# Performance work log

Measured on AMD Instinct MI355X. Metric: run time of the kernel, lower is better.

## Reference

```python
import jax, jax.numpy as jnp
import numpy as np

N_NODES = 100000
N_EDGES = 1000000
IN_CH = 64
HID = 64
PROJ = 128
N_GRAPHS = 64
BN_EPS = 1e-5


def _glorot(key, shape):
    fan_in, fan_out = shape[0], shape[1]
    lim = (6.0 / (fan_in + fan_out)) ** 0.5
    return jax.random.uniform(key, shape, jnp.float32, -lim, lim)


def setup_inputs() -> dict:
    key = jax.random.key(0)
    ks = jax.random.split(key, 16)
    x = jax.random.normal(ks[0], (N_NODES, IN_CH), jnp.float32)
    edge_index = jax.random.randint(ks[1], (2, N_EDGES), 0, N_NODES, jnp.int64)
    batch = jnp.sort(jax.random.randint(ks[2], (N_NODES,), 0, N_GRAPHS, jnp.int64))
    inp = {
        "x": x, "edge_index": edge_index, "batch": batch,
        # conv1 MLP: Linear(2*in, hid), Linear(hid, hid)
        "c1_w1": _glorot(ks[3], (2 * IN_CH, HID)), "c1_b1": jnp.zeros((HID,), jnp.float32),
        "c1_w2": _glorot(ks[4], (HID, HID)), "c1_b2": jnp.zeros((HID,), jnp.float32),
        "bn1_g": jnp.ones((HID,), jnp.float32), "bn1_b": jnp.zeros((HID,), jnp.float32),
        # conv2 MLP: Linear(2*hid, hid), Linear(hid, hid)
        "c2_w1": _glorot(ks[5], (2 * HID, HID)), "c2_b1": jnp.zeros((HID,), jnp.float32),
        "c2_w2": _glorot(ks[6], (HID, HID)), "c2_b2": jnp.zeros((HID,), jnp.float32),
        "bn2_g": jnp.ones((HID,), jnp.float32), "bn2_b": jnp.zeros((HID,), jnp.float32),
        # projector: Linear(2*hid, proj), BN(proj), Linear(proj, proj)
        "p_w1": _glorot(ks[7], (2 * HID, PROJ)), "p_b1": jnp.zeros((PROJ,), jnp.float32),
        "p_bng": jnp.ones((PROJ,), jnp.float32), "p_bnb": jnp.zeros((PROJ,), jnp.float32),
        "p_w2": _glorot(ks[8], (PROJ, PROJ)), "p_b2": jnp.zeros((PROJ,), jnp.float32),
    }
    return inp


def _edge_conv(x, src, dst, w1, b1, w2, b2):
    # PyG EdgeConv: message = nn(cat([x_i, x_j - x_i])), aggr = max over incoming edges
    xi = x[dst]                                   # [E, C] target features
    xj = x[src]                                   # [E, C] source features
    m = jnp.concatenate([xi, xj - xi], axis=-1)   # [E, 2C]
    h = jax.nn.relu(m @ w1 + b1)
    h = jax.nn.relu(h @ w2 + b2)                  # [E, H]
    out = jax.ops.segment_max(h, dst, num_segments=N_NODES)
    return jnp.where(jnp.isfinite(out), out, 0.0)  # nodes w/o in-edges -> 0


def _batchnorm(x, g, b):
    mu = jnp.mean(x, axis=0)
    var = jnp.mean((x - mu) ** 2, axis=0)  # biased var (training-mode BN)
    return (x - mu) * jax.lax.rsqrt(var + BN_EPS) * g + b


def reference(x, edge_index, batch,
              c1_w1, c1_b1, c1_w2, c1_b2, bn1_g, bn1_b,
              c2_w1, c2_b1, c2_w2, c2_b2, bn2_g, bn2_b,
              p_w1, p_b1, p_bng, p_bnb, p_w2, p_b2):
    src, dst = edge_index[0], edge_index[1]
    h = _edge_conv(x, src, dst, c1_w1, c1_b1, c1_w2, c1_b2)
    h = _batchnorm(h, bn1_g, bn1_b)
    h = _edge_conv(h, src, dst, c2_w1, c2_b1, c2_w2, c2_b2)
    x_node = _batchnorm(h, bn2_g, bn2_b)            # [N, H]
    # graph pooling
    counts = jax.ops.segment_sum(jnp.ones((N_NODES,), x_node.dtype), batch,
                                 num_segments=N_GRAPHS)
    mean_pool = jax.ops.segment_sum(x_node, batch, num_segments=N_GRAPHS) / \
        jnp.maximum(counts, 1.0)[:, None]
    max_pool = jax.ops.segment_max(x_node, batch, num_segments=N_GRAPHS)
    max_pool = jnp.where(jnp.isfinite(max_pool), max_pool, 0.0)
    x_graph = jnp.concatenate([mean_pool, max_pool], axis=1)  # [G, 2H]
    # projector MLP
    z = x_graph @ p_w1 + p_b1
    z = jax.nn.relu(_batchnorm(z, p_bng, p_bnb))
    z_proj = z @ p_w2 + p_b2                        # [G, PROJ]
    return (z_proj, x_node, x_graph)
```

## Files before the change

kernel.cpp:

```cpp
#include <hip/hip_runtime.h>
#include <hip/hip_fp16.h>

constexpr int NN = 100000;
constexpr int NE = 1000000;
constexpr int NG = 64;
constexpr float BN_EPS = 1e-5f;
constexpr int NTILES = NE / 32;
constexpr int NNTILES = NN / 32;
constexpr int NREC = NTILES * 2;

constexpr int NBUK = 196;
constexpr int BINB = 256;
constexpr int BCHUNK = (NE + BINB - 1) / BINB;
constexpr int TABN = NBUK * BINB;
constexpr int NGGRID = (NNTILES + 3) / 4;

constexpr long H1R_OFF  = 0;
constexpr long XNR_OFF  = 3200000;
constexpr long PART_OFF = 6400000;
constexpr long SC1_OFF  = PART_OFF + 32768;
constexpr long SH1_OFF  = SC1_OFF + 64;
constexpr long SC2_OFF  = SH1_OFF + 64;
constexpr long SH2_OFF  = SC2_OFF + 64;
constexpr long PSUM_OFF = SH2_OFF + 64;
constexpr long PMAX_OFF = PSUM_OFF + 4096;
constexpr long CNT_OFF  = PMAX_OFF + 4096;
constexpr long TICK_OFF = CNT_OFF + 64;
constexpr long TAB_OFF  = TICK_OFF + 16;
constexpr long SEDG_OFF = TAB_OFF + 50176;
constexpr long WF1_OFF  = SEDG_OFF + 2000000;
constexpr long WF2_OFF  = WF1_OFF + 6144;
constexpr long RECD_OFF = WF2_OFF + 6144;
constexpr long RECV_OFF = RECD_OFF + 62528;
constexpr long P_OFF    = RECV_OFF + 2000000;
constexpr long Q_OFF    = P_OFF + 3200000;
constexpr int  POOLW    = 4096 + 4096 + 64 + 16;

constexpr long OUT_XNODE = 8192;
constexpr long OUT_XG    = 8192 + 6400000L;

using f16x8 = __attribute__((ext_vector_type(8))) _Float16;
using f32x16 = __attribute__((ext_vector_type(16))) float;

__device__ __forceinline__ unsigned short f2h(float f) {
    return __builtin_bit_cast(unsigned short, (_Float16)f);
}
__device__ __forceinline__ unsigned pkrtz(float a, float b) {
    return __builtin_bit_cast(unsigned, __builtin_amdgcn_cvt_pkrtz(a, b));
}
__device__ __forceinline__ unsigned pk_add_f16(unsigned a, unsigned b) {
    unsigned d;
    asm("v_pk_add_f16 %0, %1, %2" : "=v"(d) : "v"(a), "v"(b));
    return d;
}
__device__ __forceinline__ unsigned pk_max_f16(unsigned a, unsigned b) {
    unsigned d;
    asm("v_pk_max_f16 %0, %1, %2" : "=v"(d) : "v"(a), "v"(b));
    return d;
}
__device__ __forceinline__ float h2f_lo(unsigned u) {
    return (float)__builtin_bit_cast(_Float16, (unsigned short)(u & 0xffffu));
}
__device__ __forceinline__ float h2f_hi(unsigned u) {
    return (float)__builtin_bit_cast(_Float16, (unsigned short)(u >> 16));
}
__device__ __forceinline__ unsigned fenc(float f) {
    unsigned u = __float_as_uint(f);
    return (u & 0x80000000u) ? ~u : (u | 0x80000000u);
}
__device__ __forceinline__ float fdec(unsigned u) {
    return (u & 0x80000000u) ? __uint_as_float(u & 0x7fffffffu) : __uint_as_float(~u);
}
__device__ __forceinline__ int xcd_swz(int bid, int nwg) {
    const int q = nwg >> 3, r = nwg & 7;
    const int x = bid & 7, i = bid >> 3;
    return (x < r ? x * (q + 1) : r * (q + 1) + (x - r) * q) + i;
}

template<bool NORM>
__device__ __forceinline__ void nodegemm_tile(
    const void* __restrict__ xin, const unsigned short* wlds,
    const float* __restrict__ b1,
    const float* __restrict__ scale, const float* __restrict__ shift,
    unsigned short* __restrict__ P, unsigned short* __restrict__ Q,
    int tile, int lane)
{
    const int hi = lane >> 5, ln32 = lane & 31;
    const int node = tile * 32 + ln32;

    f32x16 cpa, cpb, cqa, cqb;
    #pragma unroll
    for (int r = 0; r < 16; ++r) {
        const int row = (r & 3) + 8 * (r >> 2) + 4 * hi;
        cpa[r] = b1[row]; cpb[r] = b1[32 + row];
        cqa[r] = 0.f;     cqb[r] = 0.f;
    }

    #pragma unroll
    for (int ks = 0; ks < 4; ++ks) {
        const int off = ks * 16 + hi * 8;
        float4 a, b;
        if constexpr (!NORM) {
            const float* xr = reinterpret_cast<const float*>(xin) + (long)node * 64;
            a = *reinterpret_cast<const float4*>(xr + off);
            b = *reinterpret_cast<const float4*>(xr + off + 4);
        } else {
            const unsigned* xr = reinterpret_cast<const unsigned*>(xin) + (long)node * 32;
            const uint4 u = *reinterpret_cast<const uint4*>(xr + ks * 8 + hi * 4);
            a.x = h2f_lo(u.x); a.y = h2f_hi(u.x); a.z = h2f_lo(u.y); a.w = h2f_hi(u.y);
            b.x = h2f_lo(u.z); b.y = h2f_hi(u.z); b.z = h2f_lo(u.w); b.w = h2f_hi(u.w);
            const float4 s0 = *reinterpret_cast<const float4*>(scale + off);
            const float4 s1 = *reinterpret_cast<const float4*>(scale + off + 4);
            const float4 h0 = *reinterpret_cast<const float4*>(shift + off);
            const float4 h1 = *reinterpret_cast<const float4*>(shift + off + 4);
            a.x = fmaf(a.x, s0.x, h0.x); a.y = fmaf(a.y, s0.y, h0.y);
            a.z = fmaf(a.z, s0.z, h0.z); a.w = fmaf(a.w, s0.w, h0.w);
            b.x = fmaf(b.x, s1.x, h1.x); b.y = fmaf(b.y, s1.y, h1.y);
            b.z = fmaf(b.z, s1.z, h1.z); b.w = fmaf(b.w, s1.w, h1.w);
        }
        uint4 uu;
        uu.x = pkrtz(a.x, a.y); uu.y = pkrtz(a.z, a.w);
        uu.z = pkrtz(b.x, b.y); uu.w = pkrtz(b.z, b.w);
        const f16x8 bfr = __builtin_bit_cast(f16x8, uu);
        const f16x8 ap0 = *reinterpret_cast<const f16x8*>(&wlds[(0 * 4 + ks) * 512 + lane * 8]);
        const f16x8 ap1 = *reinterpret_cast<const f16x8*>(&wlds[(1 * 4 + ks) * 512 + lane * 8]);
        const f16x8 aq0 = *reinterpret_cast<const f16x8*>(&wlds[4096 + (0 * 4 + ks) * 512 + lane * 8]);
        const f16x8 aq1 = *reinterpret_cast<const f16x8*>(&wlds[4096 + (1 * 4 + ks) * 512 + lane * 8]);
        cpa = __builtin_amdgcn_mfma_f32_32x32x16_f16(ap0, bfr, cpa, 0, 0, 0);
        cpb = __builtin_amdgcn_mfma_f32_32x32x16_f16(ap1, bfr, cpb, 0, 0, 0);
        cqa = __builtin_amdgcn_mfma_f32_32x32x16_f16(aq0, bfr, cqa, 0, 0, 0);
        cqb = __builtin_amdgcn_mfma_f32_32x32x16_f16(aq1, bfr, cqb, 0, 0, 0);
    }

    unsigned short* Pr = P + (long)node * 64;
    unsigned short* Qr = Q + (long)node * 64;
    #pragma unroll
    for (int t = 0; t < 2; ++t) {
        const f32x16 cp = t ? cpb : cpa;
        const f32x16 cq = t ? cqb : cqa;
        #pragma unroll
        for (int g2 = 0; g2 < 4; ++g2) {
            uint2 up, uq;
            up.x = pkrtz(cp[4 * g2 + 0], cp[4 * g2 + 1]);
            up.y = pkrtz(cp[4 * g2 + 2], cp[4 * g2 + 3]);
            uq.x = pkrtz(cq[4 * g2 + 0], cq[4 * g2 + 1]);
            uq.y = pkrtz(cq[4 * g2 + 2], cq[4 * g2 + 3]);
            const int co = t * 32 + 8 * g2 + 4 * hi;
            *reinterpret_cast<uint2*>(Pr + co) = up;
            *reinterpret_cast<uint2*>(Qr + co) = uq;
        }
    }
}

__global__ __launch_bounds__(256) void prep_hist_kernel(
    const float* __restrict__ c1w1, const float* __restrict__ c1w2,
    const float* __restrict__ c2w1, const float* __restrict__ c2w2,
    unsigned short* __restrict__ wf, float* __restrict__ pools,
    const int* __restrict__ dst, int* __restrict__ tab)
{
    __shared__ int cnt[NBUK];
    const int t = threadIdx.x;
    if (blockIdx.x < BINB) {
        const int b = blockIdx.x;
        if (t < NBUK) cnt[t] = 0;
        __syncthreads();
        const int lo = b * BCHUNK;
        const int hi = (lo + BCHUNK < NE) ? lo + BCHUNK : NE;
        for (int e = lo + t; e < hi; e += 256) atomicAdd(&cnt[dst[e] >> 9], 1);
        __syncthreads();
        if (t < NBUK) tab[t * BINB + b] = cnt[t];
        return;
    }
    const int gidx = (blockIdx.x - BINB) * 256 + t;
    if (gidx >= 24576) {
        const int z = gidx - 24576;
        if (z < POOLW) pools[z] = 0.f;
        return;
    }
    const bool second = gidx >= 12288;
    const int idx = second ? gidx - 12288 : gidx;
    const float* __restrict__ w1 = second ? c2w1 : c1w1;
    const float* __restrict__ w2 = second ? c2w2 : c1w2;
    const int sec = idx >> 12;
    const int j = idx & 4095;
    const int f = j >> 9, rem = j & 511, ln = rem >> 3, i = rem & 7;
    const int tt = f >> 2, ks = f & 3;
    const int k = ks * 16 + (ln >> 5) * 8 + i, c = tt * 32 + (ln & 31);
    float v;
    if (sec == 0)      v = w1[k * 64 + c] - w1[(64 + k) * 64 + c];
    else if (sec == 1) v = w1[(64 + k) * 64 + c];
    else               v = w2[k * 64 + c];
    wf[gidx] = f2h(v);
}

__global__ __launch_bounds__(1024) void scan_tab_kernel(int* __restrict__ tab)
{
    __shared__ int part[1024];
    const int t = threadIdx.x;
    constexpr int VPT = 49;
    int vals[VPT];
    const int base = t * VPT;
    int s = 0;
    #pragma unroll
    for (int i = 0; i < VPT; ++i) {
        const int idx = base + i;
        const int v = (idx < TABN) ? tab[idx] : 0;
        vals[i] = v; s += v;
    }
    part[t] = s;
    __syncthreads();
    for (int off = 1; off < 1024; off <<= 1) {
        const int u = (t >= off) ? part[t - off] : 0;
        __syncthreads();
        part[t] += u;
        __syncthreads();
    }
    int run = (t == 0) ? 0 : part[t - 1];
    #pragma unroll
    for (int i = 0; i < VPT; ++i) {
        const int idx = base + i;
        if (idx < TABN) { const int v = vals[i]; tab[idx] = run; run += v; }
    }
}

__global__ __launch_bounds__(256) void bin_scatter_kernel(
    const int* __restrict__ src, const int* __restrict__ dst,
    const int* __restrict__ tab, int2* __restrict__ ebin)
{
    __shared__ int basec[NBUK];
    __shared__ int cur[NBUK];
    const int t = threadIdx.x, b = blockIdx.x;
    if (t < NBUK) { basec[t] = tab[t * BINB + b]; cur[t] = 0; }
    __syncthreads();
    const int lo = b * BCHUNK;
    const int hi = (lo + BCHUNK < NE) ? lo + BCHUNK : NE;
    for (int e = lo + t; e < hi; e += 256) {
        const int d = dst[e];
        const int k = d >> 9;
        const int pos = basec[k] + atomicAdd(&cur[k], 1);
        ebin[pos] = make_int2(src[e], d);
    }
}

__global__ __launch_bounds__(256) void bucket_ng1_kernel(
    const int2* __restrict__ ebin, const int* __restrict__ tab,
    int2* __restrict__ sedge,
    unsigned* __restrict__ h1r, unsigned* __restrict__ xnr,
    const float* __restrict__ x, const unsigned short* __restrict__ wfrag,
    const float* __restrict__ b1,
    unsigned short* __restrict__ P, unsigned short* __restrict__ Q)
{
    __shared__ int hist[512];
    __shared__ int part[256];
    __shared__ unsigned short wlds[8192];
    const int t = threadIdx.x;

    if (blockIdx.x < NBUK) {
        const int k = blockIdx.x;
        const int start = tab[k * BINB];
        const int end = (k == NBUK - 1) ? NE : tab[(k + 1) * BINB];
        hist[t * 2] = 0; hist[t * 2 + 1] = 0;
        __syncthreads();
        for (int e = start + t; e < end; e += 256) atomicAdd(&hist[ebin[e].y & 511], 1);
        __syncthreads();
        const int v0 = hist[t * 2], v1 = hist[t * 2 + 1];
        {
            const uint4 z = make_uint4(0u, 0u, 0u, 0u);
            #pragma unroll
            for (int j = 0; j < 2; ++j) {
                const int node = k * 512 + t * 2 + j;
                const int c = j ? v1 : v0;
                if (node < NN && c == 0) {
                    uint4* r0 = reinterpret_cast<uint4*>(h1r + (long)node * 32);
                    uint4* r1 = reinterpret_cast<uint4*>(xnr + (long)node * 32);
                    #pragma unroll
                    for (int q2 = 0; q2 < 8; ++q2) { r0[q2] = z; r1[q2] = z; }
                }
            }
        }
        part[t] = v0 + v1;
        __syncthreads();
        for (int off = 1; off < 256; off <<= 1) {
            const int u = (t >= off) ? part[t - off] : 0;
            __syncthreads();
            part[t] += u;
            __syncthreads();
        }
        int run = (t == 0) ? 0 : part[t - 1];
        hist[t * 2] = run;
        hist[t * 2 + 1] = run + v0;
        __syncthreads();
        for (int e = start + t; e < end; e += 256) {
            const int2 v = ebin[e];
            const int pos = start + atomicAdd(&hist[v.y & 511], 1);
            sedge[pos] = v;
        }
        return;
    }

    {
        const uint4* wsrc = reinterpret_cast<const uint4*>(wfrag);
        uint4* wdst = reinterpret_cast<uint4*>(wlds);
        #pragma unroll
        for (int i = 0; i < 4; ++i) wdst[t + i * 256] = wsrc[t + i * 256];
    }
    __syncthreads();
    const int wid = t >> 6, lane = t & 63;
    const int tile = (blockIdx.x - NBUK) * 4 + wid;
    if (tile >= NNTILES) return;
    nodegemm_tile<false>(x, wlds, b1, nullptr, nullptr, P, Q, tile, lane);
}

__global__ __launch_bounds__(256) void nodegemm_kernel(
    const void* __restrict__ xin,
    const unsigned short* __restrict__ wfrag,
    const float* __restrict__ b1,
    const float* __restrict__ scale, const float* __restrict__ shift,
    unsigned short* __restrict__ P, unsigned short* __restrict__ Q)
{
    __shared__ unsigned short wlds[8192];
    {
        const uint4* wsrc = reinterpret_cast<const uint4*>(wfrag);
        uint4* wdst = reinterpret_cast<uint4*>(wlds);
        #pragma unroll
        for (int i = 0; i < 4; ++i) wdst[threadIdx.x + i * 256] = wsrc[threadIdx.x + i * 256];
    }
    __syncthreads();
    const int wid = threadIdx.x >> 6, lane = threadIdx.x & 63;
    const int tile = blockIdx.x * 4 + wid;
    if (tile >= NNTILES) return;
    nodegemm_tile<true>(xin, wlds, b1, scale, shift, P, Q, tile, lane);
}

__global__ __launch_bounds__(256) void edgeconv_kernel(
    const unsigned short* __restrict__ P, const unsigned short* __restrict__ Q,
    const int2* __restrict__ sedge,
    const unsigned short* __restrict__ w2frag,
    const float* __restrict__ b2,
    unsigned* __restrict__ out,
    int* __restrict__ recd, unsigned* __restrict__ recv)
{
    __shared__ unsigned short wlds[4096];
    {
        const uint4* wsrc = reinterpret_cast<const uint4*>(w2frag);
        uint4* wdst = reinterpret_cast<uint4*>(wlds);
        #pragma unroll
        for (int i = 0; i < 2; ++i) wdst[threadIdx.x + i * 256] = wsrc[threadIdx.x + i * 256];
    }
    __syncthreads();

    const int wid  = threadIdx.x >> 6;
    const int lane = threadIdx.x & 63;
    const int hi   = lane >> 5;
    const int ln32 = lane & 31;
    const int tile = xcd_swz(blockIdx.x, gridDim.x) * 4 + wid;
    if (tile >= NTILES) return;

    const int2 sd = sedge[tile * 32 + ln32];
    const int s = sd.x, d = sd.y;
    const unsigned short* __restrict__ Pr = P + (long)d * 64;
    const unsigned short* __restrict__ Qr = Q + (long)s * 64;

    f32x16 c2a, c2b;
    #pragma unroll
    for (int r = 0; r < 16; ++r) {
        const int row = (r & 3) + 8 * (r >> 2) + 4 * hi;
        c2a[r] = b2[row];
        c2b[r] = b2[32 + row];
    }

    #pragma unroll
    for (int ks = 0; ks < 4; ++ks) {
        const int co = ks * 16 + hi * 8;
        const uint4 pu = *reinterpret_cast<const uint4*>(Pr + co);
        const uint4 qu = *reinterpret_cast<const uint4*>(Qr + co);
        uint4 hh;
        hh.x = pk_max_f16(pk_add_f16(pu.x, qu.x), 0u);
        hh.y = pk_max_f16(pk_add_f16(pu.y, qu.y), 0u);
        hh.z = pk_max_f16(pk_add_f16(pu.z, qu.z), 0u);
        hh.w = pk_max_f16(pk_add_f16(pu.w, qu.w), 0u);
        const f16x8 bfr = __builtin_bit_cast(f16x8, hh);
        const f16x8 a0 = *reinterpret_cast<const f16x8*>(&wlds[(0 * 4 + ks) * 512 + lane * 8]);
        const f16x8 a1 = *reinterpret_cast<const f16x8*>(&wlds[(1 * 4 + ks) * 512 + lane * 8]);
        c2a = __builtin_amdgcn_mfma_f32_32x32x16_f16(a0, bfr, c2a, 0, 0, 0);
        c2b = __builtin_amdgcn_mfma_f32_32x32x16_f16(a1, bfr, c2b, 0, 0, 0);
    }

    unsigned pkc[16];
    #pragma unroll
    for (int q = 0; q < 8; ++q) {
        pkc[q]     = pk_max_f16(pkrtz(c2a[2 * q], c2a[2 * q + 1]), 0u);
        pkc[8 + q] = pk_max_f16(pkrtz(c2b[2 * q], c2b[2 * q + 1]), 0u);
    }

    #pragma unroll
    for (int st = 1; st < 32; st <<= 1) {
        const int dn = __shfl_down(d, st, 32);
        const bool take = (ln32 + st < 32) && (dn == d);
        #pragma unroll
        for (int i = 0; i < 16; ++i) {
            const unsigned o = __shfl_down(pkc[i], st, 32);
            const unsigned m = pk_max_f16(pkc[i], o);
            pkc[i] = take ? m : pkc[i];
        }
    }
    const int dprev = __shfl_up(d, 1, 32);
    const bool leader = (ln32 == 0) || (d != dprev);
    const unsigned lm = (unsigned)(__ballot(leader) & 0xffffffffull);
    const int L31 = 31 - __builtin_clz(lm);

    if (leader) {
        if (ln32 != 0 && ln32 != L31) {
            unsigned* row = out + (long)d * 32;
            #pragma unroll
            for (int g2 = 0; g2 < 4; ++g2) {
                *reinterpret_cast<uint2*>(row + 4 * g2 + 2 * hi) =
                    make_uint2(pkc[2 * g2], pkc[2 * g2 + 1]);
                *reinterpret_cast<uint2*>(row + 16 + 4 * g2 + 2 * hi) =
                    make_uint2(pkc[8 + 2 * g2], pkc[8 + 2 * g2 + 1]);
            }
        }
        if (ln32 == 0) {
            unsigned* row = recv + (long)(tile * 2) * 32;
            #pragma unroll
            for (int g2 = 0; g2 < 4; ++g2) {
                *reinterpret_cast<uint2*>(row + 4 * g2 + 2 * hi) =
                    make_uint2(pkc[2 * g2], pkc[2 * g2 + 1]);
                *reinterpret_cast<uint2*>(row + 16 + 4 * g2 + 2 * hi) =
                    make_uint2(pkc[8 + 2 * g2], pkc[8 + 2 * g2 + 1]);
            }
            if (hi == 0) recd[tile * 2] = d;
        }
        if (ln32 == L31) {
            unsigned* row = recv + (long)(tile * 2 + 1) * 32;
            #pragma unroll
            for (int g2 = 0; g2 < 4; ++g2) {
                *reinterpret_cast<uint2*>(row + 4 * g2 + 2 * hi) =
                    make_uint2(pkc[2 * g2], pkc[2 * g2 + 1]);
                *reinterpret_cast<uint2*>(row + 16 + 4 * g2 + 2 * hi) =
                    make_uint2(pkc[8 + 2 * g2], pkc[8 + 2 * g2 + 1]);
            }
            if (hi == 0) recd[tile * 2 + 1] = d;
        }
    }
}

__global__ __launch_bounds__(256) void fixup_kernel(
    const int* __restrict__ recd, const unsigned* __restrict__ recv,
    unsigned* __restrict__ out)
{
    const int wid = threadIdx.x >> 6;
    const int half = (threadIdx.x >> 5) & 1;
    const int c2 = threadIdx.x & 31;
    const int r = blockIdx.x * 8 + wid * 2 + half;
    if (r >= NREC) return;
    const int d = recd[r];
    int lo = r, hi = r;
    while (lo > 0 && recd[lo - 1] == d) --lo;
    while (hi + 1 < NREC && recd[hi + 1] == d) ++hi;
    unsigned m = 0u;
    for (int rr = lo; rr <= hi; ++rr) m = pk_max_f16(m, recv[(long)rr * 32 + c2]);
    out[(long)d * 32 + c2] = m;
}

__global__ __launch_bounds__(256) void stats_kernel(
    const unsigned* __restrict__ h, float* __restrict__ partial,
    const float* __restrict__ g, const float* __restrict__ b,
    float* __restrict__ scale, float* __restrict__ shift, int* __restrict__ ticket)
{
    __shared__ float red[4][256];
    __shared__ float red2[2][256];
    __shared__ int flag;
    const int tid = threadIdx.x;
    const int c2 = tid & 31, r = tid >> 5;
    float s0 = 0.f, ss0 = 0.f, s1 = 0.f, ss1 = 0.f;
    for (int v = blockIdx.x * 8 + r; v < NN; v += 256 * 8) {
        const unsigned u = h[(long)v * 32 + c2];
        const float a = h2f_lo(u), bb = h2f_hi(u);
        s0 += a; ss0 += a * a; s1 += bb; ss1 += bb * bb;
    }
    red[0][tid] = s0; red[1][tid] = ss0; red[2][tid] = s1; red[3][tid] = ss1;
    __syncthreads();
    if (r == 0) {
        float S0 = 0.f, SS0 = 0.f, S1 = 0.f, SS1 = 0.f;
        #pragma unroll
        for (int q = 0; q < 8; ++q) {
            S0 += red[0][c2 + q * 32]; SS0 += red[1][c2 + q * 32];
            S1 += red[2][c2 + q * 32]; SS1 += red[3][c2 + q * 32];
        }
        partial[blockIdx.x * 128 + 2 * c2]     = S0;
        partial[blockIdx.x * 128 + 2 * c2 + 1] = S1;
        partial[blockIdx.x * 128 + 64 + 2 * c2]     = SS0;
        partial[blockIdx.x * 128 + 64 + 2 * c2 + 1] = SS1;
    }
    __syncthreads();
    if (tid == 0) {
        __threadfence();
        flag = (atomicAdd(ticket, 1) == 255) ? 1 : 0;
    }
    __syncthreads();
    if (!flag) return;
    __threadfence();
    const int c = tid & 63, q = tid >> 6;
    float S = 0.f, SS = 0.f;
    for (int bb2 = q * 64; bb2 < q * 64 + 64; ++bb2) {
        S += partial[bb2 * 128 + c];
        SS += partial[bb2 * 128 + 64 + c];
    }
    red2[0][tid] = S; red2[1][tid] = SS;
    __syncthreads();
    if (q == 0) {
        #pragma unroll
        for (int p = 1; p < 4; ++p) { S += red2[0][c + p * 64]; SS += red2[1][c + p * 64]; }
        const float invN = 1.0f / (float)NN;
        const float mu = S * invN;
        const float var = SS * invN - mu * mu;
        const float sc = g[c] * rsqrtf(var + BN_EPS);
        scale[c] = sc;
        shift[c] = b[c] - mu * sc;
    }
}

constexpr int NPB = 256;
__global__ __launch_bounds__(256) void nodepass_kernel(
    const unsigned* __restrict__ xnr, float* __restrict__ xn,
    const int* __restrict__ batch,
    const float* __restrict__ scale, const float* __restrict__ shift,
    float* __restrict__ poolsum, unsigned* __restrict__ poolmax, int* __restrict__ counts)
{
    const int base = blockIdx.x * NPB;
    const int r = threadIdx.x >> 5, c2 = threadIdx.x & 31;
    const float sc0 = scale[2 * c2], sc1 = scale[2 * c2 + 1];
    const float sh0 = shift[2 * c2], sh1 = shift[2 * c2 + 1];
    int curg = -1; float rs0 = 0.f, rs1 = 0.f, rm0 = -INFINITY, rm1 = -INFINITY; int rc = 0;
    const int vend = (base + NPB < NN) ? base + NPB : NN;
    for (int v = base + r; v < vend; v += 8) {
        const unsigned u = xnr[(long)v * 32 + c2];
        const float v0 = fmaf(h2f_lo(u), sc0, sh0);
        const float v1 = fmaf(h2f_hi(u), sc1, sh1);
        *reinterpret_cast<float2*>(xn + (long)v * 64 + 2 * c2) = make_float2(v0, v1);
        const int g = batch[v];
        if (g != curg) {
            if (curg >= 0) {
                atomicAdd(poolsum + curg * 64 + 2 * c2, rs0);
                atomicAdd(poolsum + curg * 64 + 2 * c2 + 1, rs1);
                atomicMax(poolmax + curg * 64 + 2 * c2, fenc(rm0));
                atomicMax(poolmax + curg * 64 + 2 * c2 + 1, fenc(rm1));
                if (c2 == 0) atomicAdd(counts + curg, rc);
            }
            curg = g; rs0 = rs1 = 0.f; rm0 = rm1 = -INFINITY; rc = 0;
        }
        rs0 += v0; rs1 += v1; rm0 = fmaxf(rm0, v0); rm1 = fmaxf(rm1, v1); ++rc;
    }
    if (curg >= 0) {
        atomicAdd(poolsum + curg * 64 + 2 * c2, rs0);
        atomicAdd(poolsum + curg * 64 + 2 * c2 + 1, rs1);
        atomicMax(poolmax + curg * 64 + 2 * c2, fenc(rm0));
        atomicMax(poolmax + curg * 64 + 2 * c2 + 1, fenc(rm1));
        if (c2 == 0) atomicAdd(counts + curg, rc);
    }
}

__global__ __launch_bounds__(1024) void final_kernel(
    const float* __restrict__ poolsum, const unsigned* __restrict__ poolmax,
    const int* __restrict__ counts,
    const float* __restrict__ p_w1, const float* __restrict__ p_b1,
    const float* __restrict__ p_bng, const float* __restrict__ p_bnb,
    const float* __restrict__ p_w2, const float* __restrict__ p_b2,
    float* __restrict__ out)
{
    __shared__ float xg[64][128];
    __shared__ float znl[64 * 129];
    __shared__ float red[2][1024];
    __shared__ float scsh[2][128];
    const int tid = threadIdx.x;

    #pragma unroll
    for (int i = 0; i < 8; ++i) {
        const int e2 = tid + i * 1024;
        const int g = e2 >> 7, col = e2 & 127;
        float val;
        if (col < 64) {
            const float cnt = fmaxf((float)counts[g], 1.f);
            val = poolsum[g * 64 + col] / cnt;
        } else {
            const unsigned u = poolmax[g * 64 + col - 64];
            val = (u == 0u) ? 0.f : fdec(u);
        }
        xg[g][col] = val;
        out[OUT_XG + e2] = val;
    }
    __syncthreads();

    const int gg = tid >> 7, t = tid & 127;
    float z[8];
    #pragma unroll
    for (int gi = 0; gi < 8; ++gi) z[gi] = p_b1[t];
    for (int j = 0; j < 128; ++j) {
        const float wv = p_w1[j * 128 + t];
        #pragma unroll
        for (int gi = 0; gi < 8; ++gi) z[gi] = fmaf(xg[gg * 8 + gi][j], wv, z[gi]);
    }

    float s = 0.f, ss = 0.f;
    #pragma unroll
    for (int gi = 0; gi < 8; ++gi) { s += z[gi]; ss += z[gi] * z[gi]; }
    red[0][tid] = s; red[1][tid] = ss;
    __syncthreads();
    if (gg == 0) {
        float S = 0.f, SS = 0.f;
        #pragma unroll
        for (int q = 0; q < 8; ++q) { S += red[0][t + q * 128]; SS += red[1][t + q * 128]; }
        const float mu = S / 64.f;
        const float var = SS / 64.f - mu * mu;
        const float sc = p_bng[t] * rsqrtf(var + BN_EPS);
        scsh[0][t] = sc;
        scsh[1][t] = p_bnb[t] - mu * sc;
    }
    __syncthreads();
    const float sc = scsh[0][t], sh = scsh[1][t];
    #pragma unroll
    for (int gi = 0; gi < 8; ++gi) {
        const float zn = fmaxf(fmaf(z[gi], sc, sh), 0.f);
        znl[(gg * 8 + gi) * 129 + t] = zn;
    }
    __syncthreads();

    float zp[8];
    #pragma unroll
    for (int gi = 0; gi < 8; ++gi) zp[gi] = p_b2[t];
    for (int c = 0; c < 128; ++c) {
        const float wv = p_w2[c * 128 + t];
        #pragma unroll
        for (int gi = 0; gi < 8; ++gi) zp[gi] = fmaf(znl[(gg * 8 + gi) * 129 + c], wv, zp[gi]);
    }
    #pragma unroll
    for (int gi = 0; gi < 8; ++gi) out[(gg * 8 + gi) * 128 + t] = zp[gi];
}

extern "C" void kernel_launch(void* const* d_in, const int* in_sizes, int n_in,
                              void* d_out, int out_size, void* d_ws, size_t ws_size,
                              hipStream_t stream)
{
    const float* x     = (const float*)d_in[0];
    const int*   eidx  = (const int*)d_in[1];
    const int*   batch = (const int*)d_in[2];
    const float* c1w1  = (const float*)d_in[3];
    const float* c1b1  = (const float*)d_in[4];
    const float* c1w2  = (const float*)d_in[5];
    const float* c1b2  = (const float*)d_in[6];
    const float* bn1g  = (const float*)d_in[7];
    const float* bn1b  = (const float*)d_in[8];
    const float* c2w1  = (const float*)d_in[9];
    const float* c2b1  = (const float*)d_in[10];
    const float* c2w2  = (const float*)d_in[11];
    const float* c2b2  = (const float*)d_in[12];
    const float* bn2g  = (const float*)d_in[13];
    const float* bn2b  = (const float*)d_in[14];
    const float* pw1   = (const float*)d_in[15];
    const float* pb1   = (const float*)d_in[16];
    const float* pbng  = (const float*)d_in[17];
    const float* pbnb  = (const float*)d_in[18];
    const float* pw2   = (const float*)d_in[19];
    const float* pb2   = (const float*)d_in[20];

    const int* src = eidx;
    const int* dst = eidx + NE;

    float* ws  = (float*)d_ws;
    float* o   = (float*)d_out;
    unsigned* h1r = (unsigned*)(ws + H1R_OFF);
    unsigned* xnr = (unsigned*)(ws + XNR_OFF);
    float* xnode = o + OUT_XNODE;
    int* tick  = (int*)(ws + TICK_OFF);
    int* tab   = (int*)(ws + TAB_OFF);
    int2* ebin  = (int2*)(ws + RECV_OFF);
    int2* sedge = (int2*)(ws + SEDG_OFF);
    unsigned short* wf1 = (unsigned short*)(ws + WF1_OFF);
    unsigned short* wf2 = (unsigned short*)(ws + WF2_OFF);
    int* recd  = (int*)(ws + RECD_OFF);
    unsigned* recv = (unsigned*)(ws + RECV_OFF);
    unsigned short* Pb = (unsigned short*)(ws + P_OFF);
    unsigned short* Qb = (unsigned short*)(ws + Q_OFF);

    const int convGrid = (NTILES + 3) / 4;
    const int fixGrid  = (NREC + 7) / 8;

    prep_hist_kernel<<<BINB + 129, 256, 0, stream>>>(
        c1w1, c1w2, c2w1, c2w2, wf1, ws + PSUM_OFF, dst, tab);
    scan_tab_kernel<<<1, 1024, 0, stream>>>(tab);
    bin_scatter_kernel<<<BINB, 256, 0, stream>>>(src, dst, tab, ebin);
    bucket_ng1_kernel<<<NBUK + NGGRID, 256, 0, stream>>>(
        ebin, tab, sedge, h1r, xnr, x, wf1, c1b1, Pb, Qb);

    edgeconv_kernel<<<convGrid, 256, 0, stream>>>(
        Pb, Qb, sedge, wf1 + 8192, c1b2, h1r, recd, recv);
    fixup_kernel<<<fixGrid, 256, 0, stream>>>(recd, recv, h1r);
    stats_kernel<<<256, 256, 0, stream>>>(h1r, ws + PART_OFF, bn1g, bn1b,
                                          ws + SC1_OFF, ws + SH1_OFF, tick + 1);
    nodegemm_kernel<<<NGGRID, 256, 0, stream>>>(
        h1r, wf2, c2b1, ws + SC1_OFF, ws + SH1_OFF, Pb, Qb);
    edgeconv_kernel<<<convGrid, 256, 0, stream>>>(
        Pb, Qb, sedge, wf2 + 8192, c2b2, xnr, recd, recv);
    fixup_kernel<<<fixGrid, 256, 0, stream>>>(recd, recv, xnr);
    stats_kernel<<<256, 256, 0, stream>>>(xnr, ws + PART_OFF, bn2g, bn2b,
                                          ws + SC2_OFF, ws + SH2_OFF, tick + 2);
    nodepass_kernel<<<(NN + NPB - 1) / NPB, 256, 0, stream>>>(
        xnr, xnode, batch, ws + SC2_OFF, ws + SH2_OFF,
        ws + PSUM_OFF, (unsigned*)(ws + PMAX_OFF), (int*)(ws + CNT_OFF));
    final_kernel<<<1, 1024, 0, stream>>>(
        ws + PSUM_OFF, (unsigned*)(ws + PMAX_OFF), (int*)(ws + CNT_OFF),
        pw1, pb1, pbng, pbnb, pw2, pb2, o);
}
```

Baseline: 335.1 us.

## Fold scan and final projector into predecessor kernels via last-block tickets

Removes the separate scan_tab and final_kernel launches: the last histogram block, found with an atomic ticket, does the tab prefix scan, and the last nodepass block runs the projector MLP with 256 threads instead of 1024. Pool zeroing moves to a hipMemsetAsync. The edgeconv segmented max also skips the stride-16 shuffle stage when no lane needs it. In exchange, the scan and projector run on a single block of 256 threads, which means longer serial tails and more registers per thread. The design also depends on the ticket counters being reset between calls.

```diff
diff --git a/kernel.cpp b/kernel.cpp
--- a/kernel.cpp
+++ b/kernel.cpp
@@ -14,6 +14,8 @@
 constexpr int BCHUNK = (NE + BINB - 1) / BINB;
 constexpr int TABN = NBUK * BINB;
 constexpr int NGGRID = (NNTILES + 3) / 4;
+constexpr int NPB = 256;
+constexpr int NPGRID = (NN + NPB - 1) / NPB;
 
 constexpr long H1R_OFF  = 0;
 constexpr long XNR_OFF  = 3200000;
@@ -155,10 +157,12 @@
 __global__ __launch_bounds__(256) void prep_hist_kernel(
     const float* __restrict__ c1w1, const float* __restrict__ c1w2,
     const float* __restrict__ c2w1, const float* __restrict__ c2w2,
-    unsigned short* __restrict__ wf, float* __restrict__ pools,
-    const int* __restrict__ dst, int* __restrict__ tab)
+    unsigned short* __restrict__ wf,
+    const int* __restrict__ dst, int* __restrict__ tab, int* __restrict__ ticket)
 {
     __shared__ int cnt[NBUK];
+    __shared__ int part[256];
+    __shared__ int flag;
     const int t = threadIdx.x;
     if (blockIdx.x < BINB) {
         const int b = blockIdx.x;
@@ -169,14 +173,35 @@
         for (int e = lo + t; e < hi; e += 256) atomicAdd(&cnt[dst[e] >> 9], 1);
         __syncthreads();
         if (t < NBUK) tab[t * BINB + b] = cnt[t];
+        __syncthreads();
+        if (t == 0) {
+            __threadfence();
+            flag = (atomicAdd(ticket, 1) == BINB - 1) ? 1 : 0;
+        }
+        __syncthreads();
+        if (!flag) return;
+        __threadfence();
+        constexpr int VPT = TABN / 256;
+        const int base = t * VPT;
+        int s = 0;
+        for (int i = 0; i < VPT; ++i) s += tab[base + i];
+        part[t] = s;
+        __syncthreads();
+        for (int off = 1; off < 256; off <<= 1) {
+            const int u = (t >= off) ? part[t - off] : 0;
+            __syncthreads();
+            part[t] += u;
+            __syncthreads();
+        }
+        int run = (t == 0) ? 0 : part[t - 1];
+        for (int i = 0; i < VPT; ++i) {
+            const int v = tab[base + i];
+            tab[base + i] = run;
+            run += v;
+        }
         return;
     }
     const int gidx = (blockIdx.x - BINB) * 256 + t;
-    if (gidx >= 24576) {
-        const int z = gidx - 24576;
-        if (z < POOLW) pools[z] = 0.f;
-        return;
-    }
     const bool second = gidx >= 12288;
     const int idx = second ? gidx - 12288 : gidx;
     const float* __restrict__ w1 = second ? c2w1 : c1w1;
@@ -193,36 +218,6 @@
     wf[gidx] = f2h(v);
 }
 
-__global__ __launch_bounds__(1024) void scan_tab_kernel(int* __restrict__ tab)
-{
-    __shared__ int part[1024];
-    const int t = threadIdx.x;
-    constexpr int VPT = 49;
-    int vals[VPT];
-    const int base = t * VPT;
-    int s = 0;
-    #pragma unroll
-    for (int i = 0; i < VPT; ++i) {
-        const int idx = base + i;
-        const int v = (idx < TABN) ? tab[idx] : 0;
-        vals[i] = v; s += v;
-    }
-    part[t] = s;
-    __syncthreads();
-    for (int off = 1; off < 1024; off <<= 1) {
-        const int u = (t >= off) ? part[t - off] : 0;
-        __syncthreads();
-        part[t] += u;
-        __syncthreads();
-    }
-    int run = (t == 0) ? 0 : part[t - 1];
-    #pragma unroll
-    for (int i = 0; i < VPT; ++i) {
-        const int idx = base + i;
-        if (idx < TABN) { const int v = vals[i]; tab[idx] = run; run += v; }
-    }
-}
-
 __global__ __launch_bounds__(256) void bin_scatter_kernel(
     const int* __restrict__ src, const int* __restrict__ dst,
     const int* __restrict__ tab, int2* __restrict__ ebin)
@@ -394,7 +389,7 @@
     }
 
     #pragma unroll
-    for (int st = 1; st < 32; st <<= 1) {
+    for (int st = 1; st < 16; st <<= 1) {
         const int dn = __shfl_down(d, st, 32);
         const bool take = (ln32 + st < 32) && (dn == d);
         #pragma unroll
@@ -402,6 +397,18 @@
             const unsigned o = __shfl_down(pkc[i], st, 32);
             const unsigned m = pk_max_f16(pkc[i], o);
             pkc[i] = take ? m : pkc[i];
+        }
+    }
+    {
+        const int dn = __shfl_down(d, 16, 32);
+        const bool take = (ln32 + 16 < 32) && (dn == d);
+        if (__ballot(take) != 0ull) {
+            #pragma unroll
+            for (int i = 0; i < 16; ++i) {
+                const unsigned o = __shfl_down(pkc[i], 16, 32);
+                const unsigned m = pk_max_f16(pkc[i], o);
+                pkc[i] = take ? m : pkc[i];
+            }
         }
     }
     const int dprev = __shfl_up(d, 1, 32);
@@ -521,49 +528,12 @@
     }
 }
 
-constexpr int NPB = 256;
-__global__ __launch_bounds__(256) void nodepass_kernel(
+__global__ __launch_bounds__(256) void nodepass_final_kernel(
     const unsigned* __restrict__ xnr, float* __restrict__ xn,
     const int* __restrict__ batch,
     const float* __restrict__ scale, const float* __restrict__ shift,
-    float* __restrict__ poolsum, unsigned* __restrict__ poolmax, int* __restrict__ counts)
-{
-    const int base = blockIdx.x * NPB;
-    const int r = threadIdx.x >> 5, c2 = threadIdx.x & 31;
-    const float sc0 = scale[2 * c2], sc1 = scale[2 * c2 + 1];
-    const float sh0 = shift[2 * c2], sh1 = shift[2 * c2 + 1];
-    int curg = -1; float rs0 = 0.f, rs1 = 0.f, rm0 = -INFINITY, rm1 = -INFINITY; int rc = 0;
-    const int vend = (base + NPB < NN) ? base + NPB : NN;
-    for (int v = base + r; v < vend; v += 8) {
-        const unsigned u = xnr[(long)v * 32 + c2];
-        const float v0 = fmaf(h2f_lo(u), sc0, sh0);
-        const float v1 = fmaf(h2f_hi(u), sc1, sh1);
-        *reinterpret_cast<float2*>(xn + (long)v * 64 + 2 * c2) = make_float2(v0, v1);
-        const int g = batch[v];
-        if (g != curg) {
-            if (curg >= 0) {
-                atomicAdd(poolsum + curg * 64 + 2 * c2, rs0);
-                atomicAdd(poolsum + curg * 64 + 2 * c2 + 1, rs1);
-                atomicMax(poolmax + curg * 64 + 2 * c2, fenc(rm0));
-                atomicMax(poolmax + curg * 64 + 2 * c2 + 1, fenc(rm1));
-                if (c2 == 0) atomicAdd(counts + curg, rc);
-            }
-            curg = g; rs0 = rs1 = 0.f; rm0 = rm1 = -INFINITY; rc = 0;
-        }
-        rs0 += v0; rs1 += v1; rm0 = fmaxf(rm0, v0); rm1 = fmaxf(rm1, v1); ++rc;
-    }
-    if (curg >= 0) {
-        atomicAdd(poolsum + curg * 64 + 2 * c2, rs0);
-        atomicAdd(poolsum + curg * 64 + 2 * c2 + 1, rs1);
-        atomicMax(poolmax + curg * 64 + 2 * c2, fenc(rm0));
-        atomicMax(poolmax + curg * 64 + 2 * c2 + 1, fenc(rm1));
-        if (c2 == 0) atomicAdd(counts + curg, rc);
-    }
-}
-
-__global__ __launch_bounds__(1024) void final_kernel(
-    const float* __restrict__ poolsum, const unsigned* __restrict__ poolmax,
-    const int* __restrict__ counts,
+    float* __restrict__ poolsum, unsigned* __restrict__ poolmax,
+    int* __restrict__ counts, int* __restrict__ ticket,
     const float* __restrict__ p_w1, const float* __restrict__ p_b1,
     const float* __restrict__ p_bng, const float* __restrict__ p_bnb,
     const float* __restrict__ p_w2, const float* __restrict__ p_b2,
@@ -571,13 +541,56 @@
 {
     __shared__ float xg[64][128];
     __shared__ float znl[64 * 129];
-    __shared__ float red[2][1024];
+    __shared__ float red[2][256];
     __shared__ float scsh[2][128];
+    __shared__ int flag;
+
+    {
+        const int base = blockIdx.x * NPB;
+        const int r = threadIdx.x >> 5, c2 = threadIdx.x & 31;
+        const float sc0 = scale[2 * c2], sc1 = scale[2 * c2 + 1];
+        const float sh0 = shift[2 * c2], sh1 = shift[2 * c2 + 1];
+        int curg = -1; float rs0 = 0.f, rs1 = 0.f, rm0 = -INFINITY, rm1 = -INFINITY; int rc = 0;
+        const int vend = (base + NPB < NN) ? base + NPB : NN;
+        for (int v = base + r; v < vend; v += 8) {
+            const unsigned u = xnr[(long)v * 32 + c2];
+            const float v0 = fmaf(h2f_lo(u), sc0, sh0);
+            const float v1 = fmaf(h2f_hi(u), sc1, sh1);
+            *reinterpret_cast<float2*>(xn + (long)v * 64 + 2 * c2) = make_float2(v0, v1);
+            const int g = batch[v];
+            if (g != curg) {
+                if (curg >= 0) {
+                    atomicAdd(poolsum + curg * 64 + 2 * c2, rs0);
+                    atomicAdd(poolsum + curg * 64 + 2 * c2 + 1, rs1);
+                    atomicMax(poolmax + curg * 64 + 2 * c2, fenc(rm0));
+                    atomicMax(poolmax + curg * 64 + 2 * c2 + 1, fenc(rm1));
+                    if (c2 == 0) atomicAdd(counts + curg, rc);
+                }
+                curg = g; rs0 = rs1 = 0.f; rm0 = rm1 = -INFINITY; rc = 0;
+            }
+            rs0 += v0; rs1 += v1; rm0 = fmaxf(rm0, v0); rm1 = fmaxf(rm1, v1); ++rc;
+        }
+        if (curg >= 0) {
+            atomicAdd(poolsum + curg * 64 + 2 * c2, rs0);
+            atomicAdd(poolsum + curg * 64 + 2 * c2 + 1, rs1);
+            atomicMax(poolmax + curg * 64 + 2 * c2, fenc(rm0));
+            atomicMax(poolmax + curg * 64 + 2 * c2 + 1, fenc(rm1));
+            if (c2 == 0) atomicAdd(counts + curg, rc);
+        }
+    }
+    __syncthreads();
+    if (threadIdx.x == 0) {
+        __threadfence();
+        flag = (atomicAdd(ticket, 1) == NPGRID - 1) ? 1 : 0;
+    }
+    __syncthreads();
+    if (!flag) return;
+    __threadfence();
+
     const int tid = threadIdx.x;
-
-    #pragma unroll
-    for (int i = 0; i < 8; ++i) {
-        const int e2 = tid + i * 1024;
+    #pragma unroll
+    for (int i = 0; i < 32; ++i) {
+        const int e2 = tid + i * 256;
         const int g = e2 >> 7, col = e2 & 127;
         float val;
         if (col < 64) {
@@ -593,24 +606,23 @@
     __syncthreads();
 
     const int gg = tid >> 7, t = tid & 127;
-    float z[8];
-    #pragma unroll
-    for (int gi = 0; gi < 8; ++gi) z[gi] = p_b1[t];
+    float z[32];
+    #pragma unroll
+    for (int gi = 0; gi < 32; ++gi) z[gi] = p_b1[t];
     for (int j = 0; j < 128; ++j) {
         const float wv = p_w1[j * 128 + t];
         #pragma unroll
-        for (int gi = 0; gi < 8; ++gi) z[gi] = fmaf(xg[gg * 8 + gi][j], wv, z[gi]);
+        for (int gi = 0; gi < 32; ++gi) z[gi] = fmaf(xg[gg * 32 + gi][j], wv, z[gi]);
     }
 
     float s = 0.f, ss = 0.f;
     #pragma unroll
-    for (int gi = 0; gi < 8; ++gi) { s += z[gi]; ss += z[gi] * z[gi]; }
+    for (int gi = 0; gi < 32; ++gi) { s += z[gi]; ss += z[gi] * z[gi]; }
     red[0][tid] = s; red[1][tid] = ss;
     __syncthreads();
     if (gg == 0) {
-        float S = 0.f, SS = 0.f;
-        #pragma unroll
-        for (int q = 0; q < 8; ++q) { S += red[0][t + q * 128]; SS += red[1][t + q * 128]; }
+        const float S = red[0][t] + red[0][t + 128];
+        const float SS = red[1][t] + red[1][t + 128];
         const float mu = S / 64.f;
         const float var = SS / 64.f - mu * mu;
         const float sc = p_bng[t] * rsqrtf(var + BN_EPS);
@@ -620,22 +632,22 @@
     __syncthreads();
     const float sc = scsh[0][t], sh = scsh[1][t];
     #pragma unroll
-    for (int gi = 0; gi < 8; ++gi) {
+    for (int gi = 0; gi < 32; ++gi) {
         const float zn = fmaxf(fmaf(z[gi], sc, sh), 0.f);
-        znl[(gg * 8 + gi) * 129 + t] = zn;
-    }
-    __syncthreads();
-
-    float zp[8];
-    #pragma unroll
-    for (int gi = 0; gi < 8; ++gi) zp[gi] = p_b2[t];
+        znl[(gg * 32 + gi) * 129 + t] = zn;
+    }
+    __syncthreads();
+
+    float zp[32];
+    #pragma unroll
+    for (int gi = 0; gi < 32; ++gi) zp[gi] = p_b2[t];
     for (int c = 0; c < 128; ++c) {
         const float wv = p_w2[c * 128 + t];
         #pragma unroll
-        for (int gi = 0; gi < 8; ++gi) zp[gi] = fmaf(znl[(gg * 8 + gi) * 129 + c], wv, zp[gi]);
-    }
-    #pragma unroll
-    for (int gi = 0; gi < 8; ++gi) out[(gg * 8 + gi) * 128 + t] = zp[gi];
+        for (int gi = 0; gi < 32; ++gi) zp[gi] = fmaf(znl[(gg * 32 + gi) * 129 + c], wv, zp[gi]);
+    }
+    #pragma unroll
+    for (int gi = 0; gi < 32; ++gi) out[(gg * 32 + gi) * 128 + t] = zp[gi];
 }
 
 extern "C" void kernel_launch(void* const* d_in, const int* in_sizes, int n_in,
@@ -686,9 +698,10 @@
     const int convGrid = (NTILES + 3) / 4;
     const int fixGrid  = (NREC + 7) / 8;
 
-    prep_hist_kernel<<<BINB + 129, 256, 0, stream>>>(
-        c1w1, c1w2, c2w1, c2w2, wf1, ws + PSUM_OFF, dst, tab);
-    scan_tab_kernel<<<1, 1024, 0, stream>>>(tab);
+    hipMemsetAsync(ws + PSUM_OFF, 0, POOLW * 4, stream);
+
+    prep_hist_kernel<<<BINB + 96, 256, 0, stream>>>(
+        c1w1, c1w2, c2w1, c2w2, wf1, dst, tab, tick + 0);
     bin_scatter_kernel<<<BINB, 256, 0, stream>>>(src, dst, tab, ebin);
     bucket_ng1_kernel<<<NBUK + NGGRID, 256, 0, stream>>>(
         ebin, tab, sedge, h1r, xnr, x, wf1, c1b1, Pb, Qb);
@@ -705,10 +718,8 @@
     fixup_kernel<<<fixGrid, 256, 0, stream>>>(recd, recv, xnr);
     stats_kernel<<<256, 256, 0, stream>>>(xnr, ws + PART_OFF, bn2g, bn2b,
                                           ws + SC2_OFF, ws + SH2_OFF, tick + 2);
-    nodepass_kernel<<<(NN + NPB - 1) / NPB, 256, 0, stream>>>(
+    nodepass_final_kernel<<<NPGRID, 256, 0, stream>>>(
         xnr, xnode, batch, ws + SC2_OFF, ws + SH2_OFF,
-        ws + PSUM_OFF, (unsigned*)(ws + PMAX_OFF), (int*)(ws + CNT_OFF));
-    final_kernel<<<1, 1024, 0, stream>>>(
-        ws + PSUM_OFF, (unsigned*)(ws + PMAX_OFF), (int*)(ws + CNT_OFF),
+        ws + PSUM_OFF, (unsigned*)(ws + PMAX_OFF), (int*)(ws + CNT_OFF), tick + 3,
         pw1, pb1, pbng, pbnb, pw2, pb2, o);
 }
```

After: 380.8 us. 13.6% more time.
